# Performance work log

Measured on AMD Instinct MI355X. Metric: run time of the kernel, lower is better.

The kernel has to match this reference:

```python
import jax, jax.numpy as jnp
import numpy as np
from jax import lax

# sRGB linear -> LMS matrix (Oklab M1)
M1 = jnp.array([[0.4122214708, 0.5363325363, 0.0514459929],
                [0.2119034982, 0.6806995451, 0.1073969566],
                [0.0883024619, 0.2817188376, 0.6299787005]], dtype=jnp.float32)
# LMS^(1/3) -> Oklab matrix (Oklab M2)
M2 = jnp.array([[0.2104542553, 0.7936177850, -0.0040720468],
                [1.9779984951, -2.4285922050, 0.4505937099],
                [0.0259040371, 0.7827717662, -0.8086757660]], dtype=jnp.float32)
_SX = jnp.array([[-1., 0., 1.], [-2., 0., 2.], [-1., 0., 1.]], dtype=jnp.float32)
_SY = jnp.array([[-1., -2., -1.], [0., 0., 0.], [1., 2., 1.]], dtype=jnp.float32)
SOBEL = jnp.stack([_SX, _SY])[:, None]  # (2,1,3,3) cross-correlation kernels

CLOSING_KERNEL = 11
CLOSING_PAD = CLOSING_KERNEL // 2
EDGE_THRESHOLD = 0.5
POST_DILATION = 2
EPS = 0.01


def _srgb_to_linear(srgb):
    srgb = jnp.clip(srgb, 0.0, 1.0)
    return jnp.where(srgb <= 0.04045, srgb / 12.92, ((srgb + 0.055) / 1.055) ** 2.4)


def _rgb_to_oklab(rgb):  # [B,3,H,W] -> [B,3,H,W]
    linear = _srgb_to_linear(rgb)
    lms = jnp.einsum('oc,bchw->bohw', M1, linear)
    lms = jnp.clip(lms, 1e-10, None) ** (1.0 / 3.0)
    return jnp.einsum('oc,bchw->bohw', M2, lms)


def _max_pool(x, k, p):  # torch max_pool2d pads with -inf implicitly
    return lax.reduce_window(x, -jnp.inf, lax.max, (1, 1, k, k), (1, 1, 1, 1),
                             [(0, 0), (0, 0), (p, p), (p, p)])


def _min_pool(x, k, p):  # -max_pool(-x): padding becomes +inf
    return lax.reduce_window(x, jnp.inf, lax.min, (1, 1, k, k), (1, 1, 1, 1),
                             [(0, 0), (0, 0), (p, p), (p, p)])


def _omni_edge(img):  # [B,C,H,W] -> [B,1,H,W]
    B, C, H, W = img.shape
    flat = img.reshape(B * C, 1, H, W)
    g = lax.conv_general_dilated(flat, SOBEL, (1, 1), [(1, 1), (1, 1)])  # [B*C,2,H,W]
    grad = (jnp.abs(g[:, 0]) + jnp.abs(g[:, 1])).reshape(B, C, H, W)
    return jnp.max(grad, axis=1, keepdims=True)


def _crevice_mask(target):
    edge_soft = jnp.clip(_omni_edge(target) / EDGE_THRESHOLD, 0.0, 1.0)
    dilated = _max_pool(edge_soft, CLOSING_KERNEL, CLOSING_PAD)
    closed = _min_pool(dilated, CLOSING_KERNEL, CLOSING_PAD)
    mask = jax.nn.relu(closed - edge_soft)
    if POST_DILATION > 0:
        dk = 2 * POST_DILATION + 1
        mask = _max_pool(mask, dk, POST_DILATION)
    return mask


def setup_inputs() -> dict:
    key = jax.random.key(0)
    k1, k2 = jax.random.split(key)
    shape = (8, 3, 1024, 1024)
    pred = jax.random.uniform(k1, shape, dtype=jnp.float32)
    target = jax.random.uniform(k2, shape, dtype=jnp.float32)
    return {"pred": pred, "target": target}


def reference(pred, target):
    crevice_mask = _crevice_mask(target)
    mask_sum = jnp.maximum(crevice_mask.sum(), 1.0)
    pred_lab = _rgb_to_oklab(pred)
    target_lab = _rgb_to_oklab(target)
    p_a, p_b = pred_lab[:, 1:2], pred_lab[:, 2:3]
    t_a, t_b = target_lab[:, 1:2], target_lab[:, 2:3]
    C_pred = jnp.sqrt(p_a ** 2 + p_b ** 2 + 1e-12)
    C_gt = jnp.sqrt(t_a ** 2 + t_b ** 2 + 1e-12)
    chroma_loss = (jnp.abs(C_pred - C_gt) * crevice_mask).sum() / mask_sum
    dot_ab = p_a * t_a + p_b * t_b
    cos_hue_diff = jnp.clip(dot_ab / (C_pred * C_gt + 1e-12), -1.0, 1.0)
    hue_loss = (jnp.clip(C_gt, EPS, None) * (1.0 - cos_hue_diff) * crevice_mask).sum() / mask_sum
    return chroma_loss + 2.0 * hue_loss
```

## Files before the change

### kernel.cpp

```cpp
#include <hip/hip_runtime.h>
#include <math.h>

#define SROWS 64
#define PCH   16
#define QCAP  1024


__device__ __forceinline__ float srgb_to_linear(float x) {
    x = fminf(fmaxf(x, 0.0f), 1.0f);
    return (x <= 0.04045f) ? x * (1.0f / 12.92f)
                           : powf((x + 0.055f) * (1.0f / 1.055f), 2.4f);
}

__device__ __forceinline__ void oklab_ab(float r, float g, float b,
                                         float& A, float& Bc) {
    r = srgb_to_linear(r);
    g = srgb_to_linear(g);
    b = srgb_to_linear(b);
    float l = 0.4122214708f * r + 0.5363325363f * g + 0.0514459929f * b;
    float m = 0.2119034982f * r + 0.6806995451f * g + 0.1073969566f * b;
    float s = 0.0883024619f * r + 0.2817188376f * g + 0.6299787005f * b;
    l = cbrtf(fmaxf(l, 1e-10f));
    m = cbrtf(fmaxf(m, 1e-10f));
    s = cbrtf(fmaxf(s, 1e-10f));
    A  = 1.9779984951f * l - 2.428592205f * m + 0.4505937099f * s;
    Bc = 0.0259040371f * l + 0.7827717662f * m - 0.808675766f  * s;
}

__device__ __forceinline__ void color_terms(const float* __restrict__ pred,
                                            const float* __restrict__ target,
                                            size_t off, size_t HWp, float m,
                                            float& sc, float& sh) {
    float pa, pb, ta, tb;
    oklab_ab(pred[off], pred[off + HWp], pred[off + 2 * HWp], pa, pb);
    oklab_ab(target[off], target[off + HWp], target[off + 2 * HWp], ta, tb);
    float Cp = sqrtf(pa * pa + pb * pb + 1e-12f);
    float Cg = sqrtf(ta * ta + tb * tb + 1e-12f);
    sc += fabsf(Cp - Cg) * m;
    float cosd = (pa * ta + pb * tb) / (Cp * Cg + 1e-12f);
    cosd = fminf(fmaxf(cosd, -1.0f), 1.0f);
    sh += fmaxf(Cg, 0.01f) * (1.0f - cosd) * m;
}


__global__ __launch_bounds__(256) void k1_edge(const float* __restrict__ target,
                                               float* __restrict__ edge,
                                               int H, int W) {
    const int WC = 62, BC = 248;
    int cb = (W + BC - 1) / BC;
    int rs = H / SROWS;
    int blk = blockIdx.x;
    int b   = blk / (cb * rs);
    int t   = blk % (cb * rs);
    int bxi = t / rs, ysi = t % rs;
    int lane = threadIdx.x & 63, wid = threadIdx.x >> 6;
    int c  = bxi * BC + wid * WC + lane - 1;
    int y0 = ysi * SROWS;
    size_t plane = (size_t)H * W;
    const float* tb = target + (size_t)b * 3 * plane;
    bool inc = (c >= 0 && c < W);
    bool store_ok = (lane >= 1 && lane <= WC && c < W);
    float* ep = edge + (size_t)b * plane + c;
    int lp = min(lane + 1, 63), lm = max(lane - 1, 0);

    float pr0, pr1, pr2, cu0, cu1, cu2;
    {
        bool ok = inc && (y0 - 1 >= 0);
        const float* p = tb + (size_t)(y0 - 1) * W + c;
        pr0 = ok ? p[0] : 0.f; pr1 = ok ? p[plane] : 0.f; pr2 = ok ? p[2 * plane] : 0.f;
    }
    {
        const float* p = tb + (size_t)y0 * W + c;
        cu0 = inc ? p[0] : 0.f; cu1 = inc ? p[plane] : 0.f; cu2 = inc ? p[2 * plane] : 0.f;
    }
#pragma unroll 2
    for (int y = y0; y < y0 + SROWS; ++y) {
        bool ok = inc && (y + 1 < H);
        const float* p = tb + (size_t)(y + 1) * W + c;
        float nx0 = ok ? p[0] : 0.f;
        float nx1 = ok ? p[plane] : 0.f;
        float nx2 = ok ? p[2 * plane] : 0.f;
        float g = 0.f;
#define SOBEL_CH(PR, CU, NX)                                              \
        {                                                                 \
            float u = PR + 2.f * CU + NX;                                 \
            float v = NX - PR;                                            \
            float up = __shfl(u, lp), um = __shfl(u, lm);                 \
            float vp = __shfl(v, lp), vm = __shfl(v, lm);                 \
            g = fmaxf(g, fabsf(up - um) + fabsf(vm + 2.f * v + vp));      \
        }
        SOBEL_CH(pr0, cu0, nx0)
        SOBEL_CH(pr1, cu1, nx1)
        SOBEL_CH(pr2, cu2, nx2)
#undef SOBEL_CH
        if (store_ok) ep[(size_t)y * W] = fminf(2.f * g, 1.f);
        pr0 = cu0; pr1 = cu1; pr2 = cu2;
        cu0 = nx0; cu1 = nx1; cu2 = nx2;
    }
}


template <int R, bool ISMAX, bool SUB_EDGE>
__global__ __launch_bounds__(256) void pool_kernel(const float* __restrict__ in,
                                                   const float* __restrict__ edge,
                                                   float* __restrict__ out,
                                                   int H, int W) {
    const int OUTW = 256 - 2 * R;
    __shared__ float s_v[PCH][256];
    int cb = (W + OUTW - 1) / OUTW;
    int rs = H / SROWS;
    int blk = blockIdx.x;
    int b   = blk / (cb * rs);
    int t   = blk % (cb * rs);
    int bxi = t / rs, ysi = t % rs;
    int tid = threadIdx.x;
    int col = bxi * OUTW - R + tid;
    int cc  = min(max(col, 0), W - 1);
    size_t base = (size_t)b * H * W;
    const float* colp = in + base + cc;
    int ys = ysi * SROWS;
    bool writer = (tid >= R) && (tid < OUTW + R) && (col < W);

    for (int ph = 0; ph < SROWS / PCH; ++ph) {
        int y0 = ys + ph * PCH;
        float w[PCH + 2 * R];
#pragma unroll
        for (int k = 0; k < PCH + 2 * R; ++k) {
            int r = min(max(y0 - R + k, 0), H - 1);
            w[k] = colp[(size_t)r * W];
        }
        float v[PCH];
#pragma unroll
        for (int k = 0; k < PCH; ++k) {
            float m = w[k];
#pragma unroll
            for (int d = 1; d <= 2 * R; ++d)
                m = ISMAX ? fmaxf(m, w[k + d]) : fminf(m, w[k + d]);
            v[k] = m;
        }
        __syncthreads();
#pragma unroll
        for (int k = 0; k < PCH; ++k) s_v[k][tid] = v[k];
        __syncthreads();
        if (writer) {
#pragma unroll
            for (int k = 0; k < PCH; ++k) {
                float m = s_v[k][tid - R];
#pragma unroll
                for (int d = 1; d <= 2 * R; ++d)
                    m = ISMAX ? fmaxf(m, s_v[k][tid - R + d])
                              : fminf(m, s_v[k][tid - R + d]);
                size_t gi = base + (size_t)(y0 + k) * W + col;
                out[gi] = SUB_EDGE ? fmaxf(m - edge[gi], 0.f) : m;
            }
        }
    }
}


__global__ __launch_bounds__(256) void k4_loss(const float* __restrict__ pred,
                                               const float* __restrict__ target,
                                               const float* __restrict__ mask0,
                                               float* __restrict__ partials,
                                               int H, int W, int nb) {
    const int R = 2, OUTW = 256 - 2 * R;
    __shared__ float s_v[PCH][256];
    __shared__ int   q_pos[QCAP];
    __shared__ float q_m[QCAP];
    __shared__ int   cnt;
    __shared__ float s_red[3][4];

    int cb = (W + OUTW - 1) / OUTW;
    int rs = H / SROWS;
    int blk = blockIdx.x;
    int b   = blk / (cb * rs);
    int t   = blk % (cb * rs);
    int bxi = t / rs, ysi = t % rs;
    int tid = threadIdx.x;
    int col = bxi * OUTW - R + tid;
    int cc  = min(max(col, 0), W - 1);
    size_t HWp  = (size_t)H * W;
    size_t base = (size_t)b * HWp;
    size_t cbase = (size_t)b * 3 * HWp;
    const float* colp = mask0 + base + cc;
    int ys = ysi * SROWS;
    bool writer = (tid >= R) && (tid < OUTW + R) && (col < W);

    float sm = 0.f, sc = 0.f, sh = 0.f;

    for (int ph = 0; ph < SROWS / PCH; ++ph) {
        int y0 = ys + ph * PCH;
        float w[PCH + 2 * R];
#pragma unroll
        for (int k = 0; k < PCH + 2 * R; ++k) {
            int r = min(max(y0 - R + k, 0), H - 1);
            w[k] = colp[(size_t)r * W];
        }
        float v[PCH];
#pragma unroll
        for (int k = 0; k < PCH; ++k) {
            float m = w[k];
#pragma unroll
            for (int d = 1; d <= 2 * R; ++d) m = fmaxf(m, w[k + d]);
            v[k] = m;
        }
        __syncthreads();
#pragma unroll
        for (int k = 0; k < PCH; ++k) s_v[k][tid] = v[k];
        if (tid == 0) cnt = 0;
        __syncthreads();
        if (writer) {
#pragma unroll
            for (int k = 0; k < PCH; ++k) {
                float m = s_v[k][tid - R];
#pragma unroll
                for (int d = 1; d <= 2 * R; ++d)
                    m = fmaxf(m, s_v[k][tid - R + d]);
                sm += m;
                if (m > 0.f) {
                    int pos = atomicAdd(&cnt, 1);
                    if (pos < QCAP) {
                        q_pos[pos] = ((y0 + k) << 16) | col;
                        q_m[pos] = m;
                    } else {
                        color_terms(pred, target,
                                    cbase + (size_t)(y0 + k) * W + col,
                                    HWp, m, sc, sh);
                    }
                }
            }
        }
        __syncthreads();
        int n = min(cnt, QCAP);
        for (int i = tid; i < n; i += 256) {
            int pk = q_pos[i];
            color_terms(pred, target,
                        cbase + (size_t)(pk >> 16) * W + (pk & 0xffff),
                        HWp, q_m[i], sc, sh);
        }
    }

#pragma unroll
    for (int off = 32; off > 0; off >>= 1) {
        sm += __shfl_down(sm, off);
        sc += __shfl_down(sc, off);
        sh += __shfl_down(sh, off);
    }
    int lane = tid & 63, wav = tid >> 6;
    __syncthreads();
    if (lane == 0) { s_red[0][wav] = sm; s_red[1][wav] = sc; s_red[2][wav] = sh; }
    __syncthreads();
    if (tid == 0) {
        float tm = 0, tc = 0, th = 0;
        for (int i = 0; i < 4; ++i) {
            tm += s_red[0][i]; tc += s_red[1][i]; th += s_red[2][i];
        }
        partials[blk]          = tm;
        partials[nb + blk]     = tc;
        partials[2 * nb + blk] = th;
    }
}

__global__ void finalize_kernel(const float* __restrict__ partials, int nb,
                                float* __restrict__ out) {
    double sm = 0.0, sc = 0.0, sh = 0.0;
    for (int i = threadIdx.x; i < nb; i += blockDim.x) {
        sm += (double)partials[i];
        sc += (double)partials[nb + i];
        sh += (double)partials[2 * nb + i];
    }
    __shared__ double red[3][256];
    red[0][threadIdx.x] = sm;
    red[1][threadIdx.x] = sc;
    red[2][threadIdx.x] = sh;
    __syncthreads();
    for (int s = blockDim.x / 2; s > 0; s >>= 1) {
        if ((int)threadIdx.x < s) {
            red[0][threadIdx.x] += red[0][threadIdx.x + s];
            red[1][threadIdx.x] += red[1][threadIdx.x + s];
            red[2][threadIdx.x] += red[2][threadIdx.x + s];
        }
        __syncthreads();
    }
    if (threadIdx.x == 0) {
        double ms = fmax(red[0][0], 1.0);
        out[0] = (float)(red[1][0] / ms + 2.0 * red[2][0] / ms);
    }
}


extern "C" void kernel_launch(void* const* d_in, const int* in_sizes, int n_in,
                              void* d_out, int out_size, void* d_ws, size_t ws_size,
                              hipStream_t stream) {
    const float* pred   = (const float*)d_in[0];
    const float* target = (const float*)d_in[1];
    float* out = (float*)d_out;

    const int H = 1024, W = 1024;
    int Bn = in_sizes[0] / (3 * H * W);
    size_t plane = (size_t)Bn * H * W * sizeof(float);

    char* ws = (char*)d_ws;
    float* planeA = (float*)ws;
    float* planeB = (float*)(ws + plane);
    float* partials = (float*)(ws + 2 * plane);

    int rs = H / SROWS;
    int cb1 = (W + 247) / 248;
    int cbP = (W + 245) / 246;
    int cb4 = (W + 251) / 252;
    int g1 = Bn * cb1 * rs;
    int gP = Bn * cbP * rs;
    int g4 = Bn * cb4 * rs;

    k1_edge<<<g1, 256, 0, stream>>>(target, planeA, H, W);
    pool_kernel<5, true, false><<<gP, 256, 0, stream>>>(planeA, nullptr, planeB, H, W);
    pool_kernel<5, false, true><<<gP, 256, 0, stream>>>(planeB, planeA, planeA, H, W);
    k4_loss<<<g4, 256, 0, stream>>>(pred, target, planeA, partials, H, W, g4);
    finalize_kernel<<<1, 256, 0, stream>>>(partials, g4, out);
}
```

Before: 109.7 us.

## Fuse dilation, erosion, subtract and post-dilation into loss kernel; vectorize edge kernel

Merges the two separable pool kernels and the loss kernel into one kernel that recomputes max-pool, min-pool, edge subtraction and the 5x5 post-dilation from the edge plane, using halo rows and columns in shared memory. This removes two full-plane intermediate writes and reads plus two launches. The edge kernel is also rewritten to process four columns per thread with float4 loads and stores over full-width rows. The price is heavy halo recomputation (32 input rows loaded per 8 output rows), more register pressure, and smaller output tiles.

New measurement: 109.7 us. About the same (+0.0%).

```diff
diff --git a/kernel.cpp b/kernel.cpp
--- a/kernel.cpp
+++ b/kernel.cpp
@@ -1,9 +1,12 @@
 #include <hip/hip_runtime.h>
 #include <math.h>
 
+#define K1_NR 16
 #define SROWS 64
-#define PCH   16
+#define PCH   8
 #define QCAP  1024
+#define OUTLO 12
+#define OUTW  232
 
 
 __device__ __forceinline__ float srgb_to_linear(float x) {
@@ -46,185 +49,198 @@
 __global__ __launch_bounds__(256) void k1_edge(const float* __restrict__ target,
                                                float* __restrict__ edge,
                                                int H, int W) {
-    const int WC = 62, BC = 248;
-    int cb = (W + BC - 1) / BC;
-    int rs = H / SROWS;
-    int blk = blockIdx.x;
-    int b   = blk / (cb * rs);
-    int t   = blk % (cb * rs);
-    int bxi = t / rs, ysi = t % rs;
-    int lane = threadIdx.x & 63, wid = threadIdx.x >> 6;
-    int c  = bxi * BC + wid * WC + lane - 1;
-    int y0 = ysi * SROWS;
-    size_t plane = (size_t)H * W;
-    const float* tb = target + (size_t)b * 3 * plane;
-    bool inc = (c >= 0 && c < W);
-    bool store_ok = (lane >= 1 && lane <= WC && c < W);
-    float* ep = edge + (size_t)b * plane + c;
-    int lp = min(lane + 1, 63), lm = max(lane - 1, 0);
-
-    float pr0, pr1, pr2, cu0, cu1, cu2;
-    {
-        bool ok = inc && (y0 - 1 >= 0);
-        const float* p = tb + (size_t)(y0 - 1) * W + c;
-        pr0 = ok ? p[0] : 0.f; pr1 = ok ? p[plane] : 0.f; pr2 = ok ? p[2 * plane] : 0.f;
-    }
-    {
-        const float* p = tb + (size_t)y0 * W + c;
-        cu0 = inc ? p[0] : 0.f; cu1 = inc ? p[plane] : 0.f; cu2 = inc ? p[2 * plane] : 0.f;
-    }
+    int strips = H / K1_NR;
+    int b   = blockIdx.x / strips;
+    int ysi = blockIdx.x % strips;
+    int lane = threadIdx.x & 63, q = threadIdx.x >> 6;
+    int C0 = q << 8;
+    int col0 = C0 + (lane << 2);
+    int y0 = ysi * K1_NR;
+    size_t HW = (size_t)H * W;
+    const float* tb = target + (size_t)b * 3 * HW;
+    float* ep = edge + (size_t)b * HW;
+
+    int hcol = (lane == 0) ? (C0 - 1) : (C0 + 256);
+    bool hen = (lane == 0 || lane == 63) && (hcol >= 0) && (hcol < W);
+    int lm = (lane + 63) & 63, lp = (lane + 1) & 63;
+
+    float4 pr[3], cu[3], nx[3];
+    float hpr[3], hcu[3], hnx[3];
+#pragma unroll
+    for (int c = 0; c < 3; ++c) {
+        const float* p = tb + (size_t)c * HW;
+        if (y0 > 0) {
+            pr[c]  = *(const float4*)(p + (size_t)(y0 - 1) * W + col0);
+            hpr[c] = hen ? p[(size_t)(y0 - 1) * W + hcol] : 0.f;
+        } else {
+            pr[c] = make_float4(0.f, 0.f, 0.f, 0.f);
+            hpr[c] = 0.f;
+        }
+        cu[c]  = *(const float4*)(p + (size_t)y0 * W + col0);
+        hcu[c] = hen ? p[(size_t)y0 * W + hcol] : 0.f;
+    }
+
 #pragma unroll 2
-    for (int y = y0; y < y0 + SROWS; ++y) {
-        bool ok = inc && (y + 1 < H);
-        const float* p = tb + (size_t)(y + 1) * W + c;
-        float nx0 = ok ? p[0] : 0.f;
-        float nx1 = ok ? p[plane] : 0.f;
-        float nx2 = ok ? p[2 * plane] : 0.f;
-        float g = 0.f;
-#define SOBEL_CH(PR, CU, NX)                                              \
-        {                                                                 \
-            float u = PR + 2.f * CU + NX;                                 \
-            float v = NX - PR;                                            \
-            float up = __shfl(u, lp), um = __shfl(u, lm);                 \
-            float vp = __shfl(v, lp), vm = __shfl(v, lm);                 \
-            g = fmaxf(g, fabsf(up - um) + fabsf(vm + 2.f * v + vp));      \
-        }
-        SOBEL_CH(pr0, cu0, nx0)
-        SOBEL_CH(pr1, cu1, nx1)
-        SOBEL_CH(pr2, cu2, nx2)
-#undef SOBEL_CH
-        if (store_ok) ep[(size_t)y * W] = fminf(2.f * g, 1.f);
-        pr0 = cu0; pr1 = cu1; pr2 = cu2;
-        cu0 = nx0; cu1 = nx1; cu2 = nx2;
-    }
-}
-
-
-template <int R, bool ISMAX, bool SUB_EDGE>
-__global__ __launch_bounds__(256) void pool_kernel(const float* __restrict__ in,
-                                                   const float* __restrict__ edge,
-                                                   float* __restrict__ out,
-                                                   int H, int W) {
-    const int OUTW = 256 - 2 * R;
-    __shared__ float s_v[PCH][256];
-    int cb = (W + OUTW - 1) / OUTW;
-    int rs = H / SROWS;
-    int blk = blockIdx.x;
-    int b   = blk / (cb * rs);
-    int t   = blk % (cb * rs);
-    int bxi = t / rs, ysi = t % rs;
-    int tid = threadIdx.x;
-    int col = bxi * OUTW - R + tid;
-    int cc  = min(max(col, 0), W - 1);
-    size_t base = (size_t)b * H * W;
-    const float* colp = in + base + cc;
-    int ys = ysi * SROWS;
-    bool writer = (tid >= R) && (tid < OUTW + R) && (col < W);
-
-    for (int ph = 0; ph < SROWS / PCH; ++ph) {
-        int y0 = ys + ph * PCH;
-        float w[PCH + 2 * R];
-#pragma unroll
-        for (int k = 0; k < PCH + 2 * R; ++k) {
-            int r = min(max(y0 - R + k, 0), H - 1);
-            w[k] = colp[(size_t)r * W];
-        }
-        float v[PCH];
-#pragma unroll
-        for (int k = 0; k < PCH; ++k) {
-            float m = w[k];
-#pragma unroll
-            for (int d = 1; d <= 2 * R; ++d)
-                m = ISMAX ? fmaxf(m, w[k + d]) : fminf(m, w[k + d]);
-            v[k] = m;
-        }
-        __syncthreads();
-#pragma unroll
-        for (int k = 0; k < PCH; ++k) s_v[k][tid] = v[k];
-        __syncthreads();
-        if (writer) {
-#pragma unroll
-            for (int k = 0; k < PCH; ++k) {
-                float m = s_v[k][tid - R];
-#pragma unroll
-                for (int d = 1; d <= 2 * R; ++d)
-                    m = ISMAX ? fmaxf(m, s_v[k][tid - R + d])
-                              : fminf(m, s_v[k][tid - R + d]);
-                size_t gi = base + (size_t)(y0 + k) * W + col;
-                out[gi] = SUB_EDGE ? fmaxf(m - edge[gi], 0.f) : m;
-            }
-        }
-    }
-}
-
-
-__global__ __launch_bounds__(256) void k4_loss(const float* __restrict__ pred,
-                                               const float* __restrict__ target,
-                                               const float* __restrict__ mask0,
-                                               float* __restrict__ partials,
-                                               int H, int W, int nb) {
-    const int R = 2, OUTW = 256 - 2 * R;
-    __shared__ float s_v[PCH][256];
+    for (int y = y0; y < y0 + K1_NR; ++y) {
+        bool okn = (y + 1 < H);
+#pragma unroll
+        for (int c = 0; c < 3; ++c) {
+            const float* p = tb + (size_t)c * HW + (size_t)(y + 1) * W;
+            nx[c]  = okn ? *(const float4*)(p + col0)
+                         : make_float4(0.f, 0.f, 0.f, 0.f);
+            hnx[c] = (okn && hen) ? p[hcol] : 0.f;
+        }
+        float4 g = make_float4(0.f, 0.f, 0.f, 0.f);
+#pragma unroll
+        for (int c = 0; c < 3; ++c) {
+            float4 u, v;
+            u.x = fmaf(2.f, cu[c].x, pr[c].x) + nx[c].x;
+            u.y = fmaf(2.f, cu[c].y, pr[c].y) + nx[c].y;
+            u.z = fmaf(2.f, cu[c].z, pr[c].z) + nx[c].z;
+            u.w = fmaf(2.f, cu[c].w, pr[c].w) + nx[c].w;
+            v.x = nx[c].x - pr[c].x;
+            v.y = nx[c].y - pr[c].y;
+            v.z = nx[c].z - pr[c].z;
+            v.w = nx[c].w - pr[c].w;
+            float hu = fmaf(2.f, hcu[c], hpr[c]) + hnx[c];
+            float hv = hnx[c] - hpr[c];
+            float um1 = __shfl(u.w, lm); if (lane == 0)  um1 = hu;
+            float up4 = __shfl(u.x, lp); if (lane == 63) up4 = hu;
+            float vm1 = __shfl(v.w, lm); if (lane == 0)  vm1 = hv;
+            float vp4 = __shfl(v.x, lp); if (lane == 63) vp4 = hv;
+            float4 gx, gy;
+            gx.x = u.y - um1; gx.y = u.z - u.x; gx.z = u.w - u.y; gx.w = up4 - u.z;
+            gy.x = fmaf(2.f, v.x, vm1) + v.y;
+            gy.y = fmaf(2.f, v.y, v.x) + v.z;
+            gy.z = fmaf(2.f, v.z, v.y) + v.w;
+            gy.w = fmaf(2.f, v.w, v.z) + vp4;
+            g.x = fmaxf(g.x, fabsf(gx.x) + fabsf(gy.x));
+            g.y = fmaxf(g.y, fabsf(gx.y) + fabsf(gy.y));
+            g.z = fmaxf(g.z, fabsf(gx.z) + fabsf(gy.z));
+            g.w = fmaxf(g.w, fabsf(gx.w) + fabsf(gy.w));
+        }
+        float4 e;
+        e.x = fminf(2.f * g.x, 1.f);
+        e.y = fminf(2.f * g.y, 1.f);
+        e.z = fminf(2.f * g.z, 1.f);
+        e.w = fminf(2.f * g.w, 1.f);
+        *(float4*)(ep + (size_t)y * W + col0) = e;
+#pragma unroll
+        for (int c = 0; c < 3; ++c) {
+            pr[c] = cu[c]; cu[c] = nx[c];
+            hpr[c] = hcu[c]; hcu[c] = hnx[c];
+        }
+    }
+}
+
+
+__global__ __launch_bounds__(256) void k234(const float* __restrict__ edge,
+                                            const float* __restrict__ pred,
+                                            const float* __restrict__ target,
+                                            float* __restrict__ partials,
+                                            int H, int W, int nb) {
+    __shared__ float bufA[22][256];
     __shared__ int   q_pos[QCAP];
     __shared__ float q_m[QCAP];
     __shared__ int   cnt;
     __shared__ float s_red[3][4];
 
-    int cb = (W + OUTW - 1) / OUTW;
-    int rs = H / SROWS;
+    int cgs = (W + OUTW - 1) / OUTW;
+    int rs  = H / SROWS;
     int blk = blockIdx.x;
-    int b   = blk / (cb * rs);
-    int t   = blk % (cb * rs);
-    int bxi = t / rs, ysi = t % rs;
+    int b   = blk / (cgs * rs);
+    int t   = blk % (cgs * rs);
+    int g   = t / rs, ysi = t % rs;
     int tid = threadIdx.x;
-    int col = bxi * OUTW - R + tid;
+    int col = g * OUTW - OUTLO + tid;
     int cc  = min(max(col, 0), W - 1);
-    size_t HWp  = (size_t)H * W;
-    size_t base = (size_t)b * HWp;
+    size_t HWp = (size_t)H * W;
+    size_t base  = (size_t)b * HWp;
     size_t cbase = (size_t)b * 3 * HWp;
-    const float* colp = mask0 + base + cc;
+    const float* ecol = edge + base + cc;
     int ys = ysi * SROWS;
-    bool writer = (tid >= R) && (tid < OUTW + R) && (col < W);
+    bool writer = (tid >= OUTLO) && (tid < OUTLO + OUTW) && (col < W);
+    int lo5 = min(max(tid - 5, 0), 245);
+    int lo2 = min(max(tid - 2, 0), 251);
 
     float sm = 0.f, sc = 0.f, sh = 0.f;
 
     for (int ph = 0; ph < SROWS / PCH; ++ph) {
-        int y0 = ys + ph * PCH;
-        float w[PCH + 2 * R];
-#pragma unroll
-        for (int k = 0; k < PCH + 2 * R; ++k) {
-            int r = min(max(y0 - R + k, 0), H - 1);
-            w[k] = colp[(size_t)r * W];
-        }
-        float v[PCH];
-#pragma unroll
-        for (int k = 0; k < PCH; ++k) {
+        int f0 = ys + ph * PCH;
+        float w[32];
+#pragma unroll
+        for (int i = 0; i < 32; ++i) {
+            int r = min(max(f0 - 12 + i, 0), H - 1);
+            w[i] = ecol[(size_t)r * W];
+        }
+        float dv[22];
+#pragma unroll
+        for (int k = 0; k < 22; ++k) {
             float m = w[k];
 #pragma unroll
-            for (int d = 1; d <= 2 * R; ++d) m = fmaxf(m, w[k + d]);
-            v[k] = m;
-        }
-        __syncthreads();
-#pragma unroll
-        for (int k = 0; k < PCH; ++k) s_v[k][tid] = v[k];
+            for (int d = 1; d <= 10; ++d) m = fmaxf(m, w[k + d]);
+            dv[k] = m;
+        }
+        __syncthreads();
+#pragma unroll
+        for (int k = 0; k < 22; ++k) bufA[k][tid] = dv[k];
+        __syncthreads();
+        float dil[22];
+#pragma unroll
+        for (int k = 0; k < 22; ++k) {
+            float m = bufA[k][lo5];
+#pragma unroll
+            for (int d = 1; d <= 10; ++d) m = fmaxf(m, bufA[k][lo5 + d]);
+            dil[k] = m;
+        }
+        float cv[12];
+#pragma unroll
+        for (int k = 0; k < 12; ++k) {
+            float m = dil[k];
+#pragma unroll
+            for (int d = 1; d <= 10; ++d) m = fminf(m, dil[k + d]);
+            cv[k] = m;
+        }
+        __syncthreads();
+#pragma unroll
+        for (int k = 0; k < 12; ++k) bufA[k][tid] = cv[k];
+        __syncthreads();
+        float msk[12];
+#pragma unroll
+        for (int k = 0; k < 12; ++k) {
+            float m = bufA[k][lo5];
+#pragma unroll
+            for (int d = 1; d <= 10; ++d) m = fminf(m, bufA[k][lo5 + d]);
+            msk[k] = fmaxf(m - w[10 + k], 0.f);
+        }
+        __syncthreads();
+#pragma unroll
+        for (int k = 0; k < 12; ++k) bufA[k][tid] = msk[k];
         if (tid == 0) cnt = 0;
         __syncthreads();
+        float hm[12];
+#pragma unroll
+        for (int k = 0; k < 12; ++k) {
+            float m = bufA[k][lo2];
+#pragma unroll
+            for (int d = 1; d <= 4; ++d) m = fmaxf(m, bufA[k][lo2 + d]);
+            hm[k] = m;
+        }
         if (writer) {
 #pragma unroll
             for (int k = 0; k < PCH; ++k) {
-                float m = s_v[k][tid - R];
-#pragma unroll
-                for (int d = 1; d <= 2 * R; ++d)
-                    m = fmaxf(m, s_v[k][tid - R + d]);
+                float m = hm[k];
+#pragma unroll
+                for (int d = 1; d <= 4; ++d) m = fmaxf(m, hm[k + d]);
                 sm += m;
                 if (m > 0.f) {
                     int pos = atomicAdd(&cnt, 1);
                     if (pos < QCAP) {
-                        q_pos[pos] = ((y0 + k) << 16) | col;
-                        q_m[pos] = m;
+                        q_pos[pos] = ((f0 + k) << 16) | col;
+                        q_m[pos]   = m;
                     } else {
                         color_terms(pred, target,
-                                    cbase + (size_t)(y0 + k) * W + col,
+                                    cbase + (size_t)(f0 + k) * W + col,
                                     HWp, m, sc, sh);
                     }
                 }
@@ -301,21 +317,14 @@
     size_t plane = (size_t)Bn * H * W * sizeof(float);
 
     char* ws = (char*)d_ws;
-    float* planeA = (float*)ws;
-    float* planeB = (float*)(ws + plane);
-    float* partials = (float*)(ws + 2 * plane);
-
-    int rs = H / SROWS;
-    int cb1 = (W + 247) / 248;
-    int cbP = (W + 245) / 246;
-    int cb4 = (W + 251) / 252;
-    int g1 = Bn * cb1 * rs;
-    int gP = Bn * cbP * rs;
-    int g4 = Bn * cb4 * rs;
+    float* planeA   = (float*)ws;
+    float* partials = (float*)(ws + plane);
+
+    int g1 = Bn * (H / K1_NR);
+    int cgs = (W + OUTW - 1) / OUTW;
+    int g2 = Bn * cgs * (H / SROWS);
 
     k1_edge<<<g1, 256, 0, stream>>>(target, planeA, H, W);
-    pool_kernel<5, true, false><<<gP, 256, 0, stream>>>(planeA, nullptr, planeB, H, W);
-    pool_kernel<5, false, true><<<gP, 256, 0, stream>>>(planeB, planeA, planeA, H, W);
-    k4_loss<<<g4, 256, 0, stream>>>(pred, target, planeA, partials, H, W, g4);
-    finalize_kernel<<<1, 256, 0, stream>>>(partials, g4, out);
-}
+    k234<<<g2, 256, 0, stream>>>(planeA, pred, target, partials, H, W, g2);
+    finalize_kernel<<<1, 256, 0, stream>>>(partials, g2, out);
+}
```

## Vectorize Sobel edge kernel with float4 columns and halo exchange

Applied to the files above, without the earlier changes.

The edge kernel now has each thread process four adjacent columns with float4 loads and stores. Each block covers a full 1024-wide row strip of 16 rows instead of a 248-column by 64-row tile. Horizontal neighbours come from lane shuffles, with edge lanes loading explicit halo columns, which removes the overlapping columns wasted by the old per-lane layout. This is meant to cut load instruction count and redundant traffic, at the cost of hardcoding W to 1024 (four waves of 256 columns) and giving up the bounds checks on loads.

Result: faster. 92.91 us (-15.3%).

```diff
diff --git a/kernel.cpp b/kernel.cpp
--- a/kernel.cpp
+++ b/kernel.cpp
@@ -1,6 +1,7 @@
 #include <hip/hip_runtime.h>
 #include <math.h>
 
+#define K1_NR 16
 #define SROWS 64
 #define PCH   16
 #define QCAP  1024
@@ -46,56 +47,87 @@
 __global__ __launch_bounds__(256) void k1_edge(const float* __restrict__ target,
                                                float* __restrict__ edge,
                                                int H, int W) {
-    const int WC = 62, BC = 248;
-    int cb = (W + BC - 1) / BC;
-    int rs = H / SROWS;
-    int blk = blockIdx.x;
-    int b   = blk / (cb * rs);
-    int t   = blk % (cb * rs);
-    int bxi = t / rs, ysi = t % rs;
-    int lane = threadIdx.x & 63, wid = threadIdx.x >> 6;
-    int c  = bxi * BC + wid * WC + lane - 1;
-    int y0 = ysi * SROWS;
-    size_t plane = (size_t)H * W;
-    const float* tb = target + (size_t)b * 3 * plane;
-    bool inc = (c >= 0 && c < W);
-    bool store_ok = (lane >= 1 && lane <= WC && c < W);
-    float* ep = edge + (size_t)b * plane + c;
-    int lp = min(lane + 1, 63), lm = max(lane - 1, 0);
-
-    float pr0, pr1, pr2, cu0, cu1, cu2;
-    {
-        bool ok = inc && (y0 - 1 >= 0);
-        const float* p = tb + (size_t)(y0 - 1) * W + c;
-        pr0 = ok ? p[0] : 0.f; pr1 = ok ? p[plane] : 0.f; pr2 = ok ? p[2 * plane] : 0.f;
-    }
-    {
-        const float* p = tb + (size_t)y0 * W + c;
-        cu0 = inc ? p[0] : 0.f; cu1 = inc ? p[plane] : 0.f; cu2 = inc ? p[2 * plane] : 0.f;
-    }
+    int strips = H / K1_NR;
+    int b   = blockIdx.x / strips;
+    int ysi = blockIdx.x % strips;
+    int lane = threadIdx.x & 63, q = threadIdx.x >> 6;
+    int C0 = q << 8;
+    int col0 = C0 + (lane << 2);
+    int y0 = ysi * K1_NR;
+    size_t HW = (size_t)H * W;
+    const float* tb = target + (size_t)b * 3 * HW;
+    float* ep = edge + (size_t)b * HW;
+
+    int hcol = (lane == 0) ? (C0 - 1) : (C0 + 256);
+    bool hen = (lane == 0 || lane == 63) && (hcol >= 0) && (hcol < W);
+    int lm = (lane + 63) & 63, lp = (lane + 1) & 63;
+
+    float4 pr[3], cu[3], nx[3];
+    float hpr[3], hcu[3], hnx[3];
+#pragma unroll
+    for (int c = 0; c < 3; ++c) {
+        const float* p = tb + (size_t)c * HW;
+        if (y0 > 0) {
+            pr[c]  = *(const float4*)(p + (size_t)(y0 - 1) * W + col0);
+            hpr[c] = hen ? p[(size_t)(y0 - 1) * W + hcol] : 0.f;
+        } else {
+            pr[c] = make_float4(0.f, 0.f, 0.f, 0.f);
+            hpr[c] = 0.f;
+        }
+        cu[c]  = *(const float4*)(p + (size_t)y0 * W + col0);
+        hcu[c] = hen ? p[(size_t)y0 * W + hcol] : 0.f;
+    }
+
 #pragma unroll 2
-    for (int y = y0; y < y0 + SROWS; ++y) {
-        bool ok = inc && (y + 1 < H);
-        const float* p = tb + (size_t)(y + 1) * W + c;
-        float nx0 = ok ? p[0] : 0.f;
-        float nx1 = ok ? p[plane] : 0.f;
-        float nx2 = ok ? p[2 * plane] : 0.f;
-        float g = 0.f;
-#define SOBEL_CH(PR, CU, NX)                                              \
-        {                                                                 \
-            float u = PR + 2.f * CU + NX;                                 \
-            float v = NX - PR;                                            \
-            float up = __shfl(u, lp), um = __shfl(u, lm);                 \
-            float vp = __shfl(v, lp), vm = __shfl(v, lm);                 \
-            g = fmaxf(g, fabsf(up - um) + fabsf(vm + 2.f * v + vp));      \
-        }
-        SOBEL_CH(pr0, cu0, nx0)
-        SOBEL_CH(pr1, cu1, nx1)
-        SOBEL_CH(pr2, cu2, nx2)
-#undef SOBEL_CH
-        if (store_ok) ep[(size_t)y * W] = fminf(2.f * g, 1.f);
-        pr0 = cu0; pr1 = cu1; pr2 = cu2;
-        cu0 = nx0; cu1 = nx1; cu2 = nx2;
+    for (int y = y0; y < y0 + K1_NR; ++y) {
+        bool okn = (y + 1 < H);
+#pragma unroll
+        for (int c = 0; c < 3; ++c) {
+            const float* p = tb + (size_t)c * HW + (size_t)(y + 1) * W;
+            nx[c]  = okn ? *(const float4*)(p + col0)
+                         : make_float4(0.f, 0.f, 0.f, 0.f);
+            hnx[c] = (okn && hen) ? p[hcol] : 0.f;
+        }
+        float4 g = make_float4(0.f, 0.f, 0.f, 0.f);
+#pragma unroll
+        for (int c = 0; c < 3; ++c) {
+            float4 u, v;
+            u.x = fmaf(2.f, cu[c].x, pr[c].x) + nx[c].x;
+            u.y = fmaf(2.f, cu[c].y, pr[c].y) + nx[c].y;
+            u.z = fmaf(2.f, cu[c].z, pr[c].z) + nx[c].z;
+            u.w = fmaf(2.f, cu[c].w, pr[c].w) + nx[c].w;
+            v.x = nx[c].x - pr[c].x;
+            v.y = nx[c].y - pr[c].y;
+            v.z = nx[c].z - pr[c].z;
+            v.w = nx[c].w - pr[c].w;
+            float hu = fmaf(2.f, hcu[c], hpr[c]) + hnx[c];
+            float hv = hnx[c] - hpr[c];
+            float um1 = __shfl(u.w, lm); if (lane == 0)  um1 = hu;
+            float up4 = __shfl(u.x, lp); if (lane == 63) up4 = hu;
+            float vm1 = __shfl(v.w, lm); if (lane == 0)  vm1 = hv;
+            float vp4 = __shfl(v.x, lp); if (lane == 63) vp4 = hv;
+            float4 gx, gy;
+            gx.x = u.y - um1; gx.y = u.z - u.x; gx.z = u.w - u.y; gx.w = up4 - u.z;
+            gy.x = fmaf(2.f, v.x, vm1) + v.y;
+            gy.y = fmaf(2.f, v.y, v.x) + v.z;
+            gy.z = fmaf(2.f, v.z, v.y) + v.w;
+            gy.w = fmaf(2.f, v.w, v.z) + vp4;
+            g.x = fmaxf(g.x, fabsf(gx.x) + fabsf(gy.x));
+            g.y = fmaxf(g.y, fabsf(gx.y) + fabsf(gy.y));
+            g.z = fmaxf(g.z, fabsf(gx.z) + fabsf(gy.z));
+            g.w = fmaxf(g.w, fabsf(gx.w) + fabsf(gy.w));
+        }
+        float4 e;
+        e.x = fminf(2.f * g.x, 1.f);
+        e.y = fminf(2.f * g.y, 1.f);
+        e.z = fminf(2.f * g.z, 1.f);
+        e.w = fminf(2.f * g.w, 1.f);
+        *(float4*)(ep + (size_t)y * W + col0) = e;
+#pragma unroll
+        for (int c = 0; c < 3; ++c) {
+            pr[c] = cu[c]; cu[c] = nx[c];
+            hpr[c] = hcu[c]; hcu[c] = hnx[c];
+        }
     }
 }
 
@@ -305,11 +337,10 @@
     float* planeB = (float*)(ws + plane);
     float* partials = (float*)(ws + 2 * plane);
 
+    int g1 = Bn * (H / K1_NR);
     int rs = H / SROWS;
-    int cb1 = (W + 247) / 248;
     int cbP = (W + 245) / 246;
     int cb4 = (W + 251) / 252;
-    int g1 = Bn * cb1 * rs;
     int gP = Bn * cbP * rs;
     int g4 = Bn * cb4 * rs;
 
```

## Rewrite Sobel edge kernel with float4 row-pair tiles and XCD block swizzle

Applied to the files above, without the earlier changes.

The edge kernel drops the column-strip, 64-row streaming design that used wavefront shuffles. Each block now handles two full rows: every thread loads float4 vectors from four input rows per channel plus the two halo scalars, computes Sobel for two output rows in registers, and writes float4 results. Block IDs are remapped in chunks of eight, presumably so neighbouring rows land on the same XCD and share L2 for the overlapping halo rows. In exchange, each output row pair rereads four input rows (2x vertical read amplification), and the code hardcodes W=4*256.

Result: faster. 99.54 us (-9.2%).

```diff
diff --git a/kernel.cpp b/kernel.cpp
--- a/kernel.cpp
+++ b/kernel.cpp
@@ -45,58 +45,74 @@
 
 __global__ __launch_bounds__(256) void k1_edge(const float* __restrict__ target,
                                                float* __restrict__ edge,
-                                               int H, int W) {
-    const int WC = 62, BC = 248;
-    int cb = (W + BC - 1) / BC;
-    int rs = H / SROWS;
-    int blk = blockIdx.x;
-    int b   = blk / (cb * rs);
-    int t   = blk % (cb * rs);
-    int bxi = t / rs, ysi = t % rs;
-    int lane = threadIdx.x & 63, wid = threadIdx.x >> 6;
-    int c  = bxi * BC + wid * WC + lane - 1;
-    int y0 = ysi * SROWS;
-    size_t plane = (size_t)H * W;
-    const float* tb = target + (size_t)b * 3 * plane;
-    bool inc = (c >= 0 && c < W);
-    bool store_ok = (lane >= 1 && lane <= WC && c < W);
-    float* ep = edge + (size_t)b * plane + c;
-    int lp = min(lane + 1, 63), lm = max(lane - 1, 0);
-
-    float pr0, pr1, pr2, cu0, cu1, cu2;
-    {
-        bool ok = inc && (y0 - 1 >= 0);
-        const float* p = tb + (size_t)(y0 - 1) * W + c;
-        pr0 = ok ? p[0] : 0.f; pr1 = ok ? p[plane] : 0.f; pr2 = ok ? p[2 * plane] : 0.f;
-    }
-    {
-        const float* p = tb + (size_t)y0 * W + c;
-        cu0 = inc ? p[0] : 0.f; cu1 = inc ? p[plane] : 0.f; cu2 = inc ? p[2 * plane] : 0.f;
-    }
-#pragma unroll 2
-    for (int y = y0; y < y0 + SROWS; ++y) {
-        bool ok = inc && (y + 1 < H);
-        const float* p = tb + (size_t)(y + 1) * W + c;
-        float nx0 = ok ? p[0] : 0.f;
-        float nx1 = ok ? p[plane] : 0.f;
-        float nx2 = ok ? p[2 * plane] : 0.f;
-        float g = 0.f;
-#define SOBEL_CH(PR, CU, NX)                                              \
-        {                                                                 \
-            float u = PR + 2.f * CU + NX;                                 \
-            float v = NX - PR;                                            \
-            float up = __shfl(u, lp), um = __shfl(u, lm);                 \
-            float vp = __shfl(v, lp), vm = __shfl(v, lm);                 \
-            g = fmaxf(g, fabsf(up - um) + fabsf(vm + 2.f * v + vp));      \
-        }
-        SOBEL_CH(pr0, cu0, nx0)
-        SOBEL_CH(pr1, cu1, nx1)
-        SOBEL_CH(pr2, cu2, nx2)
-#undef SOBEL_CH
-        if (store_ok) ep[(size_t)y * W] = fminf(2.f * g, 1.f);
-        pr0 = cu0; pr1 = cu1; pr2 = cu2;
-        cu0 = nx0; cu1 = nx1; cu2 = nx2;
-    }
+                                               int H, int W, int nblk) {
+    int bid = blockIdx.x;
+    if ((nblk & 7) == 0) {
+        int chunk = nblk >> 3;
+        bid = (bid & 7) * chunk + (bid >> 3);
+    }
+    int pairs = H >> 1;
+    int b  = bid / pairs;
+    int y0 = (bid % pairs) << 1;
+    int t  = threadIdx.x;
+    int col0 = t << 2;
+    size_t HW = (size_t)H * W;
+    const float* tb = target + (size_t)b * 3 * HW;
+    float* ep = edge + (size_t)b * HW + col0;
+
+    bool lok = (col0 > 0);
+    bool rok = (col0 + 4 < W);
+
+    float4 gA = make_float4(0.f, 0.f, 0.f, 0.f);
+    float4 gB = make_float4(0.f, 0.f, 0.f, 0.f);
+
+#pragma unroll
+    for (int c = 0; c < 3; ++c) {
+        const float* p = tb + (size_t)c * HW;
+        float w[4][6];
+#pragma unroll
+        for (int r = 0; r < 4; ++r) {
+            int y = y0 - 1 + r;
+            bool oky = (y >= 0) && (y < H);
+            const float* rowp = p + (size_t)y * W;
+            float4 M = oky ? *(const float4*)(rowp + col0)
+                           : make_float4(0.f, 0.f, 0.f, 0.f);
+            w[r][0] = (oky && lok) ? rowp[col0 - 1] : 0.f;
+            w[r][5] = (oky && rok) ? rowp[col0 + 4] : 0.f;
+            w[r][1] = M.x; w[r][2] = M.y; w[r][3] = M.z; w[r][4] = M.w;
+        }
+        float uA[6], vA[6], uB[6], vB[6];
+#pragma unroll
+        for (int j = 0; j < 6; ++j) {
+            uA[j] = fmaf(2.f, w[1][j], w[0][j]) + w[2][j];
+            vA[j] = w[2][j] - w[0][j];
+            uB[j] = fmaf(2.f, w[2][j], w[1][j]) + w[3][j];
+            vB[j] = w[3][j] - w[1][j];
+        }
+        float gxA[4], gyA[4], gxB[4], gyB[4];
+#pragma unroll
+        for (int i = 0; i < 4; ++i) {
+            gxA[i] = uA[i + 2] - uA[i];
+            gyA[i] = fmaf(2.f, vA[i + 1], vA[i]) + vA[i + 2];
+            gxB[i] = uB[i + 2] - uB[i];
+            gyB[i] = fmaf(2.f, vB[i + 1], vB[i]) + vB[i + 2];
+        }
+        gA.x = fmaxf(gA.x, fabsf(gxA[0]) + fabsf(gyA[0]));
+        gA.y = fmaxf(gA.y, fabsf(gxA[1]) + fabsf(gyA[1]));
+        gA.z = fmaxf(gA.z, fabsf(gxA[2]) + fabsf(gyA[2]));
+        gA.w = fmaxf(gA.w, fabsf(gxA[3]) + fabsf(gyA[3]));
+        gB.x = fmaxf(gB.x, fabsf(gxB[0]) + fabsf(gyB[0]));
+        gB.y = fmaxf(gB.y, fabsf(gxB[1]) + fabsf(gyB[1]));
+        gB.z = fmaxf(gB.z, fabsf(gxB[2]) + fabsf(gyB[2]));
+        gB.w = fmaxf(gB.w, fabsf(gxB[3]) + fabsf(gyB[3]));
+    }
+    float4 eA, eB;
+    eA.x = fminf(2.f * gA.x, 1.f); eA.y = fminf(2.f * gA.y, 1.f);
+    eA.z = fminf(2.f * gA.z, 1.f); eA.w = fminf(2.f * gA.w, 1.f);
+    eB.x = fminf(2.f * gB.x, 1.f); eB.y = fminf(2.f * gB.y, 1.f);
+    eB.z = fminf(2.f * gB.z, 1.f); eB.w = fminf(2.f * gB.w, 1.f);
+    *(float4*)(ep + (size_t)y0 * W)       = eA;
+    *(float4*)(ep + (size_t)(y0 + 1) * W) = eB;
 }
 
 
@@ -305,15 +321,14 @@
     float* planeB = (float*)(ws + plane);
     float* partials = (float*)(ws + 2 * plane);
 
+    int g1 = Bn * (H / 2);
     int rs = H / SROWS;
-    int cb1 = (W + 247) / 248;
     int cbP = (W + 245) / 246;
     int cb4 = (W + 251) / 252;
-    int g1 = Bn * cb1 * rs;
     int gP = Bn * cbP * rs;
     int g4 = Bn * cb4 * rs;
 
-    k1_edge<<<g1, 256, 0, stream>>>(target, planeA, H, W);
+    k1_edge<<<g1, 256, 0, stream>>>(target, planeA, H, W, g1);
     pool_kernel<5, true, false><<<gP, 256, 0, stream>>>(planeA, nullptr, planeB, H, W);
     pool_kernel<5, false, true><<<gP, 256, 0, stream>>>(planeB, planeA, planeA, H, W);
     k4_loss<<<g4, 256, 0, stream>>>(pred, target, planeA, partials, H, W, g4);
```
